# Kernel optimization log

Measured on AMD Instinct MI355X. Metric: run time of the kernel, lower is better.

## Reference

```python
import jax, jax.numpy as jnp
import numpy as np

EPS = 1e-5
DN = ('NCHW', 'OIHW', 'NCHW')

def conv(x, w, b, stride, pad):
    y = jax.lax.conv_general_dilated(x, w, (stride, stride), [(pad, pad), (pad, pad)], dimension_numbers=DN)
    return y + b[None, :, None, None]

def instance_norm(x, gamma, beta):
    # normalize over spatial dims per (N, C)
    mu = jnp.mean(x, axis=(2, 3), keepdims=True)
    var = jnp.var(x, axis=(2, 3), keepdims=True)
    xh = (x - mu) * jax.lax.rsqrt(var + EPS)
    return xh * gamma[None, :, None, None] + beta[None, :, None, None]

def lrelu(x):
    return jnp.where(x >= 0, x, 0.2 * x)

def block(x, w, b, g, be, stride, pad):
    return lrelu(instance_norm(conv(x, w, b, stride, pad), g, be))

def setup_inputs() -> dict:
    key = jax.random.key(0)
    ks = jax.random.split(key, 16)
    dim = 64
    def rn(k, shape, s=0.05):
        return jax.random.normal(k, shape, dtype=jnp.float32) * s
    inp = {
        'x':   jax.random.normal(ks[0], (256, 3, 64, 64), dtype=jnp.float32),
        'w1': rn(ks[1], (dim, 3, 5, 5)),        'b1': jnp.zeros((dim,), jnp.float32),
        'g1': jnp.ones((dim,), jnp.float32),    'be1': jnp.zeros((dim,), jnp.float32),
        'w2': rn(ks[2], (dim*2, dim, 5, 5)),    'b2': jnp.zeros((dim*2,), jnp.float32),
        'g2': jnp.ones((dim*2,), jnp.float32),  'be2': jnp.zeros((dim*2,), jnp.float32),
        'w3': rn(ks[3], (dim*4, dim*2, 5, 5)),  'b3': jnp.zeros((dim*4,), jnp.float32),
        'g3': jnp.ones((dim*4,), jnp.float32),  'be3': jnp.zeros((dim*4,), jnp.float32),
        'w4': rn(ks[4], (dim*4, dim*4, 3, 3)),  'b4': jnp.zeros((dim*4,), jnp.float32),
        'g4': jnp.ones((dim*4,), jnp.float32),  'be4': jnp.zeros((dim*4,), jnp.float32),
        # MBD tensor T: (in_features=4096, out_features=64, kernel_dims=50), init N(0,1)
        'T':  jax.random.normal(ks[5], (4096, 64, 50), dtype=jnp.float32),
        'fc_w': rn(ks[6], (1000, 4096 + 64), s=0.02),
        'fc_b': jnp.zeros((1000,), jnp.float32),
    }
    return inp

def reference(x, w1, b1, g1, be1, w2, b2, g2, be2, w3, b3, g3, be3, w4, b4, g4, be4, T, fc_w, fc_b):
    bs = x.shape[0]
    f = block(x, w1, b1, g1, be1, 2, 2)   # (bs,64,32,32)
    f = block(f, w2, b2, g2, be2, 2, 2)   # (bs,128,16,16)
    f = block(f, w3, b3, g3, be3, 2, 2)   # (bs,256,8,8)
    f = block(f, w4, b4, g4, be4, 2, 1)   # (bs,256,4,4)
    feat = f.reshape(bs, -1)              # (bs,4096)
    # minibatch discrimination
    M = jnp.einsum('bi,iok->bok', feat, T)          # (bs,64,50)
    norm = jnp.sum(jnp.abs(M[None] - M[:, None]), axis=3)  # (bs,bs,64); [i,j]=|M_i-M_j|
    o_b = jnp.sum(jnp.exp(-norm), axis=0) - 1.0     # (bs,64)
    mb = jnp.concatenate([feat, o_b], axis=1)       # (bs,4160)
    y = mb @ fc_w.T + fc_b                          # (bs,1000)
    return feat, y
```

## Files before the change

### kernel.cpp

```cpp
#include <hip/hip_runtime.h>
#include <hip/hip_fp16.h>
#include <math.h>

#define EPSF 1e-5f

typedef __attribute__((ext_vector_type(4))) float  floatx4;
typedef __attribute__((ext_vector_type(4))) short  short4v;
typedef __attribute__((ext_vector_type(8))) short  short8v;

__device__ __forceinline__ unsigned short cvt_bf16(float f){
  unsigned u = __float_as_uint(f);
  unsigned r = (u + 0x7FFFu + ((u >> 16) & 1u)) >> 16;
  return (unsigned short)r;
}
__device__ __forceinline__ float bf2f(unsigned short h){
  return __uint_as_float(((unsigned)h) << 16);
}
__device__ __forceinline__ short8v ld_frag(const unsigned short* p){
  short4v lo = *(const short4v*)p;
  short4v hi = *(const short4v*)(p + 4);
  return __builtin_shufflevector(lo, hi, 0,1,2,3,4,5,6,7);
}
__device__ __forceinline__ float lrelu(float x){ return x >= 0.f ? x : 0.2f*x; }

__global__ __launch_bounds__(256) void prep_k(const float* __restrict__ w1, const float* __restrict__ w2,
                                              const float* __restrict__ w3, const float* __restrict__ w4,
                                              unsigned short* __restrict__ wb1, unsigned short* __restrict__ wb2,
                                              unsigned short* __restrict__ wb3, unsigned short* __restrict__ wb4,
                                              float* __restrict__ SQ){
  int b = blockIdx.x, t = threadIdx.x;
  if (b < 32){
    int idx = b*256 + t;
    int j = idx&7, lane = (idx>>3)&63, ks = (idx>>9)&3, grp = idx>>11;
    int co = grp*16 + (lane&15);
    int k = ks*32 + ((lane>>4)<<3) + j;
    int tap6 = k>>2, ci = k&3;
    int kh = tap6/6, kw = tap6 - kh*6;
    float v = 0.f;
    if (ci < 3 && kh < 5 && kw < 5) v = w1[(co*3 + ci)*25 + kh*5 + kw];
    wb1[idx] = cvt_bf16(v);
  } else if (b < 832){
    int idx = (b-32)*256 + t;
    int grp = idx/25600, rem = idx - grp*25600;
    int tap = rem/1024, rem2 = rem - tap*1024;
    int ccg = rem2>>9, lane = (rem2>>3)&63, j = rem2&7;
    int co = grp*16 + (lane&15);
    int ci = ccg*32 + ((lane>>4)<<3) + j;
    wb2[idx] = cvt_bf16(w2[(co*64 + ci)*25 + tap]);
  } else if (b < 4032){
    int idx = (b-832)*256 + t;
    int grp = idx/51200, rem = idx - grp*51200;
    int tap = rem/2048, rem2 = rem - tap*2048;
    int ccg = rem2>>9, lane = (rem2>>3)&63, j = rem2&7;
    int co = grp*16 + (lane&15);
    int ci = ccg*32 + ((lane>>4)<<3) + j;
    wb3[idx] = cvt_bf16(w3[(co*128 + ci)*25 + tap]);
  } else if (b < 6336){
    int idx = (b-4032)*256 + t;
    int grp = idx/36864, rem = idx - grp*36864;
    int tap = rem/4096, rem2 = rem - tap*4096;
    int ccg = rem2>>9, lane = (rem2>>3)&63, j = rem2&7;
    int co = grp*16 + (lane&15);
    int ci = ccg*32 + ((lane>>4)<<3) + j;
    wb4[idx] = cvt_bf16(w4[(co*256 + ci)*9 + tap]);
  } else {
    int idx = (b-6336)*256 + t;
    SQ[idx] = 0.f;
  }
}

__global__ __launch_bounds__(256) void conv1_k(const float* __restrict__ x, const unsigned short* __restrict__ wb1P,
                                               float* __restrict__ S1, float* __restrict__ Q1,
                                               unsigned short* __restrict__ f1raw){
  const int t = threadIdx.x, n = blockIdx.x>>1, half = blockIdx.x&1;
  const int w = t>>6, lane = t&63, q = lane>>4, l16 = lane&15;
  __shared__ __align__(16) unsigned short img[36*68*4];
  short8v bf[4][4];
  #pragma unroll
  for (int nt=0;nt<4;nt++)
    #pragma unroll
    for (int ks=0;ks<4;ks++)
      bf[nt][ks] = *(const short8v*)&wb1P[((nt*4+ks)*64 + lane)*8];
  for (int i=t; i<4896; i+=256) ((unsigned*)img)[i] = 0u;
  __syncthreads();
  for (int idx=t; idx<1680; idx+=256){
    int ci = idx/560, rem = idx - ci*560;
    int tih = rem>>4, iw4 = (rem&15)<<2;
    int ih = half*32 - 2 + tih;
    if ((unsigned)ih < 64u){
      float4 v = *(const float4*)&x[((n*3+ci)<<12) + (ih<<6) + iw4];
      int base = (tih*68 + iw4 + 2)*4 + ci;
      img[base]    = cvt_bf16(v.x);
      img[base+4]  = cvt_bf16(v.y);
      img[base+8]  = cvt_bf16(v.z);
      img[base+12] = cvt_bf16(v.w);
    }
  }
  __syncthreads();
  floatx4 acc[8][4];
  #pragma unroll
  for (int mi=0;mi<8;mi++)
    #pragma unroll
    for (int nt=0;nt<4;nt++) acc[mi][nt] = (floatx4){0.f,0.f,0.f,0.f};
  #pragma unroll
  for (int mi=0; mi<8; mi++){
    int r = w*8 + mi;
    int ohl = r>>1, ow = ((r&1)<<4) + l16;
    #pragma unroll
    for (int ks=0; ks<4; ks++){
      int t0 = ks*8 + 2*q;
      int kh = t0/6, kw = t0 - kh*6;
      short8v a = ld_frag(&img[((ohl*2+kh)*68 + ow*2 + kw)*4]);
      #pragma unroll
      for (int nt=0; nt<4; nt++)
        acc[mi][nt] = __builtin_amdgcn_mfma_f32_16x16x32_bf16(a, bf[nt][ks], acc[mi][nt], 0,0,0);
    }
  }
  float sreg[4] = {0,0,0,0}, qreg[4] = {0,0,0,0};
  #pragma unroll
  for (int mi=0;mi<8;mi++){
    int r = w*8 + mi;
    #pragma unroll
    for (int nt=0;nt<4;nt++)
      #pragma unroll
      for (int e=0;e<4;e++){
        float v = acc[mi][nt][e];
        sreg[nt] += v; qreg[nt] += v*v;
        int px = half*512 + (r<<4) + (q<<2) + e;
        f1raw[(((n<<10)+px)<<6) + (nt<<4) + l16] = cvt_bf16(v);
      }
  }
  #pragma unroll
  for (int nt=0;nt<4;nt++){
    float s = sreg[nt], qq = qreg[nt];
    s  += __shfl_xor(s,16,64);  s  += __shfl_xor(s,32,64);
    qq += __shfl_xor(qq,16,64); qq += __shfl_xor(qq,32,64);
    if (q==0){
      atomicAdd(&S1[(n<<6) + (nt<<4) + l16], s);
      atomicAdd(&Q1[(n<<6) + (nt<<4) + l16], qq);
    }
  }
}

__global__ __launch_bounds__(256) void conv2_k(const unsigned short* __restrict__ fin,
                                               const unsigned short* __restrict__ wbP,
                                               const float* __restrict__ S1, const float* __restrict__ Q1,
                                               const float* __restrict__ g1, const float* __restrict__ be1,
                                               float* __restrict__ S2, float* __restrict__ Q2,
                                               unsigned short* __restrict__ fout){
  const int t = threadIdx.x;
  const int n = blockIdx.x >> 1, half = blockIdx.x & 1;
  const int w = t>>6, lane = t&63, q = lane>>4, l16 = lane&15;
  const int rw = w&1, cw = w>>1;
  __shared__ __align__(16) unsigned short tile[684*40];
  __shared__ float gmA[64], btA[64];
  if (t < 64){
    float S = S1[(n<<6)+t], Q = Q1[(n<<6)+t];
    float mu = S*(1.f/1024.f), var = fmaxf(Q*(1.f/1024.f) - mu*mu, 0.f);
    float r = rsqrtf(var+EPSF)*g1[t];
    gmA[t] = r; btA[t] = be1[t] - mu*r;
  }
  __syncthreads();
  floatx4 acc[4][4];
  #pragma unroll
  for (int mt=0;mt<4;mt++)
    #pragma unroll
    for (int nt=0;nt<4;nt++) acc[mt][nt] = (floatx4){0.f,0.f,0.f,0.f};
  int cellb[4];
  #pragma unroll
  for (int mt=0;mt<4;mt++){
    int r = rw*64 + mt*16 + l16;
    int ohl = r>>4, ow = r&15;
    cellb[mt] = (2*ohl)*36 + 2*ow;
  }
  for (int ccg = 0; ccg < 2; ccg++){
    const int cc = ccg<<5;
    if (ccg) __syncthreads();
    #pragma unroll
    for (int it=0; it<11; it++){
      int idx = it*256 + t;
      if (idx < 2736){
        int cell = idx>>2, ci0 = (idx&3)<<3;
        int tih = cell/36, tiw = cell - tih*36;
        int ih = half*16 + tih - 2, iw = tiw - 2;
        uint4 v = {0u,0u,0u,0u};
        if ((unsigned)ih < 32u && (unsigned)iw < 32u){
          v = *(const uint4*)&fin[(((n*32+ih)*32 + iw)<<6) + cc + ci0];
          unsigned short* hp = (unsigned short*)&v;
          #pragma unroll
          for (int jj=0;jj<8;jj++){
            int c = cc + ci0 + jj;
            hp[jj] = cvt_bf16(lrelu(bf2f(hp[jj])*gmA[c]+btA[c]));
          }
        }
        *(uint4*)&tile[cell*40 + ci0] = v;
      }
    }
    __syncthreads();
    const unsigned short* bp[4];
    #pragma unroll
    for (int nt=0;nt<4;nt++)
      bp[nt] = wbP + ((((cw*4+nt)*25)*2 + ccg)<<9) + lane*8;
    short8v bcur[4];
    #pragma unroll
    for (int nt=0;nt<4;nt++) bcur[nt] = *(const short8v*)bp[nt];
    for (int tap=0; tap<25; tap++){
      int tn = tap+1 < 25 ? tap+1 : tap;
      short8v bnx[4];
      #pragma unroll
      for (int nt=0;nt<4;nt++) bnx[nt] = *(const short8v*)(bp[nt] + (tn<<10));
      int kh = tap/5, kw = tap - kh*5;
      int aoff = kh*36 + kw;
      short8v a[4];
      #pragma unroll
      for (int mt=0;mt<4;mt++) a[mt] = *(const short8v*)&tile[(cellb[mt]+aoff)*40 + q*8];
      #pragma unroll
      for (int mt=0;mt<4;mt++)
        #pragma unroll
        for (int nt=0;nt<4;nt++)
          acc[mt][nt] = __builtin_amdgcn_mfma_f32_16x16x32_bf16(a[mt], bcur[nt], acc[mt][nt], 0,0,0);
      #pragma unroll
      for (int nt=0;nt<4;nt++) bcur[nt] = bnx[nt];
    }
  }
  #pragma unroll
  for (int nt=0;nt<4;nt++){
    int co = cw*64 + nt*16 + l16;
    float s=0.f, qq=0.f;
    #pragma unroll
    for (int mt=0;mt<4;mt++)
      #pragma unroll
      for (int e=0;e<4;e++){ float xv = acc[mt][nt][e]; s += xv; qq += xv*xv; }
    s  += __shfl_xor(s,16,64);  s  += __shfl_xor(s,32,64);
    qq += __shfl_xor(qq,16,64); qq += __shfl_xor(qq,32,64);
    if (q == 0){
      atomicAdd(&S2[n*128 + co], s);
      atomicAdd(&Q2[n*128 + co], qq);
    }
    #pragma unroll
    for (int mt=0;mt<4;mt++)
      #pragma unroll
      for (int e=0;e<4;e++){
        int px = half*128 + rw*64 + mt*16 + q*4 + e;
        fout[((n<<8) + px)*128 + co] = cvt_bf16(acc[mt][nt][e]);
      }
  }
}

__global__ __launch_bounds__(256) void conv3_k(const unsigned short* __restrict__ fin,
                                               const unsigned short* __restrict__ wbP,
                                               const float* __restrict__ S2, const float* __restrict__ Q2,
                                               const float* __restrict__ g2, const float* __restrict__ be2,
                                               const float* __restrict__ g, const float* __restrict__ be,
                                               unsigned short* __restrict__ fout){
  const int t = threadIdx.x, n = blockIdx.x, co0 = blockIdx.y<<7;
  const int w = t>>6, lane = t&63, q = lane>>4, l16 = lane&15;
  const int rw = w&1, cw = w>>1;
  __shared__ __align__(16) unsigned short tile[361*40];
  __shared__ float gmA[128], btA[128];
  __shared__ float SQs[2][128], SQq[2][128];
  if (t < 128){
    float S = S2[n*128+t], Q = Q2[n*128+t];
    float mu = S*(1.f/256.f), var = fmaxf(Q*(1.f/256.f) - mu*mu, 0.f);
    float r = rsqrtf(var+EPSF)*g2[t];
    gmA[t] = r; btA[t] = be2[t] - mu*r;
  }
  __syncthreads();
  floatx4 acc[2][4];
  #pragma unroll
  for (int mt=0;mt<2;mt++)
    #pragma unroll
    for (int nt=0;nt<4;nt++) acc[mt][nt] = (floatx4){0.f,0.f,0.f,0.f};
  int cellb[2];
  #pragma unroll
  for (int mt=0;mt<2;mt++){
    int r = rw*32 + mt*16 + l16;
    int oh = r>>3, ow = r&7;
    cellb[mt] = (2*oh)*19 + 2*ow;
  }
  for (int ccg = 0; ccg < 4; ccg++){
    const int cc = ccg<<5;
    if (ccg) __syncthreads();
    #pragma unroll
    for (int it=0; it<6; it++){
      int idx = it*256 + t;
      if (idx < 1444){
        int cell = idx>>2, ci0 = (idx&3)<<3;
        int tih = cell/19, tiw = cell - tih*19;
        int ih = tih - 2, iw = tiw - 2;
        uint4 v = {0u,0u,0u,0u};
        if ((unsigned)ih < 16u && (unsigned)iw < 16u){
          v = *(const uint4*)&fin[(((n*16+ih)*16 + iw)<<7) + cc + ci0];
          unsigned short* hp = (unsigned short*)&v;
          #pragma unroll
          for (int jj=0;jj<8;jj++){
            int c = cc + ci0 + jj;
            hp[jj] = cvt_bf16(lrelu(bf2f(hp[jj])*gmA[c]+btA[c]));
          }
        }
        *(uint4*)&tile[cell*40 + ci0] = v;
      }
    }
    __syncthreads();
    const unsigned short* bp[4];
    #pragma unroll
    for (int nt=0;nt<4;nt++)
      bp[nt] = wbP + (((((co0>>4)+cw*4+nt)*25)*4 + ccg)<<9) + lane*8;
    short8v bcur[4];
    #pragma unroll
    for (int nt=0;nt<4;nt++) bcur[nt] = *(const short8v*)bp[nt];
    for (int tap=0; tap<25; tap++){
      int tn = tap+1 < 25 ? tap+1 : tap;
      short8v bnx[4];
      #pragma unroll
      for (int nt=0;nt<4;nt++) bnx[nt] = *(const short8v*)(bp[nt] + (tn<<11));
      int kh = tap/5, kw = tap - kh*5;
      int aoff = kh*19 + kw;
      short8v a[2];
      #pragma unroll
      for (int mt=0;mt<2;mt++) a[mt] = *(const short8v*)&tile[(cellb[mt]+aoff)*40 + q*8];
      #pragma unroll
      for (int mt=0;mt<2;mt++)
        #pragma unroll
        for (int nt=0;nt<4;nt++)
          acc[mt][nt] = __builtin_amdgcn_mfma_f32_16x16x32_bf16(a[mt], bcur[nt], acc[mt][nt], 0,0,0);
      #pragma unroll
      for (int nt=0;nt<4;nt++) bcur[nt] = bnx[nt];
    }
  }
  #pragma unroll
  for (int nt=0;nt<4;nt++){
    int lcol = cw*64 + nt*16 + l16;
    float s=0.f, qq=0.f;
    #pragma unroll
    for (int mt=0;mt<2;mt++)
      #pragma unroll
      for (int e=0;e<4;e++){ float xv = acc[mt][nt][e]; s += xv; qq += xv*xv; }
    s  += __shfl_xor(s,16,64);  s  += __shfl_xor(s,32,64);
    qq += __shfl_xor(qq,16,64); qq += __shfl_xor(qq,32,64);
    if (q == 0){ SQs[rw][lcol] = s; SQq[rw][lcol] = qq; }
  }
  __syncthreads();
  #pragma unroll
  for (int nt=0;nt<4;nt++){
    int lcol = cw*64 + nt*16 + l16, co = co0 + lcol;
    float S = SQs[0][lcol] + SQs[1][lcol];
    float Q = SQq[0][lcol] + SQq[1][lcol];
    float mu = S*(1.f/64.f), var = fmaxf(Q*(1.f/64.f) - mu*mu, 0.f);
    float gmv = rsqrtf(var+EPSF)*g[co];
    float btv = be[co] - mu*gmv;
    #pragma unroll
    for (int mt=0;mt<2;mt++)
      #pragma unroll
      for (int e=0;e<4;e++){
        int row = rw*32 + mt*16 + q*4 + e;
        fout[((n<<6) + row)*256 + co] = cvt_bf16(lrelu(acc[mt][nt][e]*gmv+btv));
      }
  }
}

__global__ __launch_bounds__(256) void conv4_k(const unsigned short* __restrict__ fin,
                                               const unsigned short* __restrict__ wbP,
                                               const float* __restrict__ g, const float* __restrict__ be,
                                               float* __restrict__ feat, unsigned short* __restrict__ featb){
  const int t = threadIdx.x;
  const int n0 = blockIdx.x << 1, co0 = blockIdx.y << 6;
  const int w = t>>6, lane = t&63, q = lane>>4, l16 = lane&15;
  const int rw = w&1, cw = w>>1;
  __shared__ __align__(16) unsigned short tile[2*81*40];
  floatx4 acc[2];
  acc[0] = (floatx4){0.f,0.f,0.f,0.f};
  acc[1] = (floatx4){0.f,0.f,0.f,0.f};
  const int oh = l16>>2, ow = l16&3;
  const int cellb = (2*oh)*9 + 2*ow;
  for (int ccg = 0; ccg < 8; ccg++){
    const int cc = ccg<<5;
    if (ccg) __syncthreads();
    #pragma unroll
    for (int it=0; it<3; it++){
      int idx = it*256 + t;
      if (idx < 648){
        int img = idx >= 324 ? 1 : 0;
        int rem = idx - img*324;
        int cell = rem>>2, ci0 = (rem&3)<<3;
        int tih = cell/9, tiw = cell - tih*9;
        int ih = tih - 1, iw = tiw - 1;
        uint4 v = {0u,0u,0u,0u};
        if ((unsigned)ih < 8u && (unsigned)iw < 8u)
          v = *(const uint4*)&fin[((((n0+img)*8+ih)*8 + iw)<<8) + cc + ci0];
        *(uint4*)&tile[(img*81+cell)*40 + ci0] = v;
      }
    }
    __syncthreads();
    const unsigned short* bp[2];
    #pragma unroll
    for (int nt=0;nt<2;nt++)
      bp[nt] = wbP + (((((co0>>4)+cw*2+nt)*9)*8 + ccg)<<9) + lane*8;
    short8v bcur[2];
    #pragma unroll
    for (int nt=0;nt<2;nt++) bcur[nt] = *(const short8v*)bp[nt];
    for (int tap=0; tap<9; tap++){
      int tn = tap+1 < 9 ? tap+1 : tap;
      short8v bnx[2];
      #pragma unroll
      for (int nt=0;nt<2;nt++) bnx[nt] = *(const short8v*)(bp[nt] + (tn<<12));
      int kh = tap/3, kw = tap - kh*3;
      short8v a = *(const short8v*)&tile[(rw*81 + cellb + kh*9 + kw)*40 + q*8];
      #pragma unroll
      for (int nt=0;nt<2;nt++)
        acc[nt] = __builtin_amdgcn_mfma_f32_16x16x32_bf16(a, bcur[nt], acc[nt], 0,0,0);
      bcur[0] = bnx[0]; bcur[1] = bnx[1];
    }
  }
  const int nn = n0 + rw;
  #pragma unroll
  for (int nt=0;nt<2;nt++){
    int co = co0 + cw*32 + nt*16 + l16;
    float s=0.f, qq=0.f;
    #pragma unroll
    for (int e=0;e<4;e++){ float xv = acc[nt][e]; s += xv; qq += xv*xv; }
    s  += __shfl_xor(s,16,64);  s  += __shfl_xor(s,32,64);
    qq += __shfl_xor(qq,16,64); qq += __shfl_xor(qq,32,64);
    float mu = s*(1.f/16.f), var = fmaxf(qq*(1.f/16.f) - mu*mu, 0.f);
    float gmv = rsqrtf(var+EPSF)*g[co];
    float btv = be[co] - mu*gmv;
    #pragma unroll
    for (int e=0;e<4;e++){
      int px = q*4 + e;
      float vv = lrelu(acc[nt][e]*gmv+btv);
      feat [(nn<<12) + (co<<4) + px] = vv;
      featb[(nn<<12) + (co<<4) + px] = cvt_bf16(vv);
    }
  }
}

__global__ __launch_bounds__(256) void gemmM_k(const unsigned short* __restrict__ A,
                                               const float* __restrict__ T,
                                               float* __restrict__ Cp){
  const int t = threadIdx.x;
  const int n0 = blockIdx.x<<7, b0 = blockIdx.y<<7, k0 = blockIdx.z<<9;
  const int w = t>>6, lane = t&63, q = lane>>4, l16 = lane&15;
  const int rw = w&1, cw = w>>1;
  __shared__ __align__(16) unsigned short Asm[128*40];
  __shared__ __align__(16) unsigned short Bsm[128*40];
  floatx4 acc[4][4];
  #pragma unroll
  for (int mt=0;mt<4;mt++)
    #pragma unroll
    for (int nt=0;nt<4;nt++) acc[mt][nt] = (floatx4){0.f,0.f,0.f,0.f};
  for (int kk=0; kk<512; kk+=32){
    if (kk) __syncthreads();
    #pragma unroll
    for (int m=0;m<2;m++){
      int idx = t + (m<<8);
      int row = idx>>2, seg = idx&3;
      uint4 v = *(const uint4*)&A[(b0+row)*4096 + k0 + kk + (seg<<3)];
      *(uint4*)&Asm[row*40 + (seg<<3)] = v;
    }
    #pragma unroll
    for (int m=0;m<4;m++){
      int idx = t + (m<<8);
      int kr = idx>>5, ns = (idx&31)<<2;
      float4 v = *(const float4*)&T[(k0+kk+kr)*3200 + n0 + ns];
      Bsm[(ns+0)*40 + kr] = cvt_bf16(v.x);
      Bsm[(ns+1)*40 + kr] = cvt_bf16(v.y);
      Bsm[(ns+2)*40 + kr] = cvt_bf16(v.z);
      Bsm[(ns+3)*40 + kr] = cvt_bf16(v.w);
    }
    __syncthreads();
    short8v af[4], bfr[4];
    #pragma unroll
    for (int mt=0;mt<4;mt++) af[mt] = *(const short8v*)&Asm[((rw<<6)+(mt<<4)+l16)*40 + (q<<3)];
    #pragma unroll
    for (int nt=0;nt<4;nt++) bfr[nt] = *(const short8v*)&Bsm[((cw<<6)+(nt<<4)+l16)*40 + (q<<3)];
    #pragma unroll
    for (int mt=0;mt<4;mt++)
      #pragma unroll
      for (int nt=0;nt<4;nt++)
        acc[mt][nt] = __builtin_amdgcn_mfma_f32_16x16x32_bf16(af[mt], bfr[nt], acc[mt][nt], 0,0,0);
  }
  float* C = Cp + blockIdx.z * 819200;
  #pragma unroll
  for (int mt=0;mt<4;mt++)
    #pragma unroll
    for (int nt=0;nt<4;nt++)
      #pragma unroll
      for (int e=0;e<4;e++){
        int row = b0 + (rw<<6) + (mt<<4) + (q<<2) + e;
        int col = n0 + (cw<<6) + (nt<<4) + l16;
        C[row*3200 + col] = acc[mt][nt][e];
      }
}

__global__ __launch_bounds__(256) void reduceM_k(const float* __restrict__ Cp, __half* __restrict__ Mh){
  int idx = blockIdx.x*256 + threadIdx.x;
  if (idx >= 851968) return;
  int i = idx / 3328, r = idx - i*3328;
  int o = r / 52, k = r - o*52;
  float v = 0.f;
  if (k < 50){
    int src = i*3200 + o*50 + k;
    #pragma unroll
    for (int s = 0; s < 8; s++) v += Cp[s*819200 + src];
  }
  Mh[idx] = __float2half(v);
}

__global__ __launch_bounds__(256) void pair_k(const __half* __restrict__ Mh,
                                              float* __restrict__ ob, unsigned short* __restrict__ obb){
  const int j = blockIdx.x, t = threadIdx.x;
  __shared__ __align__(16) __half2 Mj[1664];
  __shared__ float red[256];
  for (int k=t; k<1664; k+=256) Mj[k] = *(const __half2*)&Mh[j*3328 + (k<<1)];
  __syncthreads();
  const int o = t & 63, ss = t >> 6;
  const __half2* mjp = &Mj[o*26];
  float sum = 0.f;
  for (int i = ss<<6; i < (ss<<6)+64; i++){
    const __half2* mip = (const __half2*)&Mh[i*3328 + o*52];
    __half2 acch = __float2half2_rn(0.f);
    #pragma unroll
    for (int k2=0;k2<26;k2++){
      __half2 d = __hsub2(mip[k2], mjp[k2]);
      acch = __hadd2(acch, __habs2(d));
    }
    float dsum = __low2float(acch) + __high2float(acch);
    sum += __expf(-dsum);
  }
  red[(o<<2)+ss] = sum;
  __syncthreads();
  if (t < 64){
    float v = red[t<<2] + red[(t<<2)+1] + red[(t<<2)+2] + red[(t<<2)+3] - 1.0f;
    ob[(j<<6)+t] = v;
    obb[(j<<6)+t] = cvt_bf16(v);
  }
}

__global__ __launch_bounds__(256) void gemmFC_k(const unsigned short* __restrict__ featb,
                                                const unsigned short* __restrict__ obb,
                                                const float* __restrict__ W, float* __restrict__ Cp){
  const int t = threadIdx.x;
  const int o0 = blockIdx.x<<7, b0 = blockIdx.y<<7, k0 = blockIdx.z*320;
  const int w = t>>6, lane = t&63, q = lane>>4, l16 = lane&15;
  const int rw = w&1, cw = w>>1;
  __shared__ __align__(16) unsigned short Asm[128*40];
  __shared__ __align__(16) unsigned short Bsm[128*40];
  floatx4 acc[4][4];
  #pragma unroll
  for (int mt=0;mt<4;mt++)
    #pragma unroll
    for (int nt=0;nt<4;nt++) acc[mt][nt] = (floatx4){0.f,0.f,0.f,0.f};
  for (int kk=0; kk<320; kk+=32){
    if (kk) __syncthreads();
    #pragma unroll
    for (int m=0;m<2;m++){
      int idx = t + (m<<8);
      int row = idx>>2, seg = idx&3;
      int i = k0 + kk + (seg<<3);
      uint4 v;
      if (i < 4096) v = *(const uint4*)&featb[(b0+row)*4096 + i];
      else          v = *(const uint4*)&obb[(b0+row)*64 + (i-4096)];
      *(uint4*)&Asm[row*40 + (seg<<3)] = v;
    }
    #pragma unroll
    for (int m=0;m<4;m++){
      int idx = t + (m<<8);
      int orow = idx>>3, seg = idx&7;
      int oo = o0 + orow;
      float4 v = {0,0,0,0};
      if (oo < 1000) v = *(const float4*)&W[oo*4160 + k0 + kk + (seg<<2)];
      unsigned short h[4] = {cvt_bf16(v.x), cvt_bf16(v.y), cvt_bf16(v.z), cvt_bf16(v.w)};
      *(uint2*)&Bsm[orow*40 + (seg<<2)] = *(uint2*)h;
    }
    __syncthreads();
    short8v af[4], bfr[4];
    #pragma unroll
    for (int mt=0;mt<4;mt++) af[mt] = *(const short8v*)&Asm[((rw<<6)+(mt<<4)+l16)*40 + (q<<3)];
    #pragma unroll
    for (int nt=0;nt<4;nt++) bfr[nt] = *(const short8v*)&Bsm[((cw<<6)+(nt<<4)+l16)*40 + (q<<3)];
    #pragma unroll
    for (int mt=0;mt<4;mt++)
      #pragma unroll
      for (int nt=0;nt<4;nt++)
        acc[mt][nt] = __builtin_amdgcn_mfma_f32_16x16x32_bf16(af[mt], bfr[nt], acc[mt][nt], 0,0,0);
  }
  float* C = Cp + blockIdx.z * 256000;
  #pragma unroll
  for (int mt=0;mt<4;mt++)
    #pragma unroll
    for (int nt=0;nt<4;nt++)
      #pragma unroll
      for (int e=0;e<4;e++){
        int row = b0 + (rw<<6) + (mt<<4) + (q<<2) + e;
        int col = o0 + (cw<<6) + (nt<<4) + l16;
        if (col < 1000) C[row*1000 + col] = acc[mt][nt][e];
      }
}

__global__ __launch_bounds__(256) void reduceY_k(const float* __restrict__ Cp, const float* __restrict__ bias,
                                                 float* __restrict__ y){
  int idx = blockIdx.x * 256 + threadIdx.x;
  if (idx >= 256000) return;
  int o = idx % 1000;
  float r = bias[o];
  #pragma unroll
  for (int s = 0; s < 13; s++) r += Cp[s*256000 + idx];
  y[idx] = r;
}

extern "C" void kernel_launch(void* const* d_in, const int* in_sizes, int n_in,
                              void* d_out, int out_size, void* d_ws, size_t ws_size,
                              hipStream_t stream){
  const float* x   = (const float*)d_in[0];
  const float* w1  = (const float*)d_in[1];
  const float* g1  = (const float*)d_in[3];
  const float* be1 = (const float*)d_in[4];
  const float* w2  = (const float*)d_in[5];
  const float* g2  = (const float*)d_in[7];
  const float* be2 = (const float*)d_in[8];
  const float* w3  = (const float*)d_in[9];
  const float* g3  = (const float*)d_in[11];
  const float* be3 = (const float*)d_in[12];
  const float* w4  = (const float*)d_in[13];
  const float* g4  = (const float*)d_in[15];
  const float* be4 = (const float*)d_in[16];
  const float* T   = (const float*)d_in[17];
  const float* fcw = (const float*)d_in[18];
  const float* fcb = (const float*)d_in[19];
  float* out = (float*)d_out;
  float* ws  = (float*)d_ws;

  unsigned short* f1raw = (unsigned short*)ws;
  unsigned short* f2    = (unsigned short*)(ws + 8388608);
  unsigned short* f3    = (unsigned short*)(ws + 12582912);
  unsigned short* featb = (unsigned short*)(ws + 14680064);
  unsigned short* wb1   = (unsigned short*)(ws + 15204352);
  unsigned short* wb2   = (unsigned short*)(ws + 15208448);
  unsigned short* wb3   = (unsigned short*)(ws + 15310848);
  unsigned short* wb4   = (unsigned short*)(ws + 15720448);
  float* S1    = ws + 16015360;
  float* Q1    = ws + 16031744;
  float* S2    = ws + 16048128;
  float* Q2    = ws + 16080896;
  float* Mp    = ws + 16113664;
  __half* Mh   = (__half*)(ws + 22667264);
  float* obuf  = ws + 23093248;
  unsigned short* obb = (unsigned short*)(ws + 23109632);
  float* yp    = ws + 23117824;
  float* feat  = out;
  float* y     = out + 1048576;

  prep_k<<<dim3(6720), 256, 0, stream>>>(w1, w2, w3, w4, wb1, wb2, wb3, wb4, S1);

  conv1_k<<<dim3(512),     256, 0, stream>>>(x, wb1, S1, Q1, f1raw);
  conv2_k<<<dim3(512),     256, 0, stream>>>(f1raw, wb2, S1, Q1, g1, be1, S2, Q2, f2);
  conv3_k<<<dim3(256, 2),  256, 0, stream>>>(f2, wb3, S2, Q2, g2, be2, g3, be3, f3);
  conv4_k<<<dim3(128, 4),  256, 0, stream>>>(f3, wb4, g4, be4, feat, featb);

  gemmM_k  <<<dim3(25, 2, 8),  256, 0, stream>>>(featb, T, Mp);
  reduceM_k<<<dim3(3328),      256, 0, stream>>>(Mp, Mh);
  pair_k   <<<dim3(256),       256, 0, stream>>>(Mh, obuf, obb);
  gemmFC_k <<<dim3(8, 2, 13),  256, 0, stream>>>(featb, obb, fcw, yp);
  reduceY_k<<<dim3(1000),      256, 0, stream>>>(yp, fcb, y);
}
```

Measured before the change: 367.2 us.

## Prepack T and fc weights into MFMA fragment layout, drop LDS staging

Adds packT_k and packW_k kernels that convert T and fc_w to bf16 in the exact per-lane MFMA fragment order, reusing dead workspace regions (f1raw, Mp). gemmM_k and gemmFC_k then load A and B fragments directly from global memory without shared-memory staging or barriers, and without per-tile fp32-to-bf16 conversion and transposed scalar LDS stores. This costs two extra launches and a full extra read/write pass over T (about 52 MB in) and fc_w each call. The GEMMs also lose LDS reuse, so each fragment is fetched from global or L2 by more waves.

```diff
diff --git a/kernel.cpp b/kernel.cpp
--- a/kernel.cpp
+++ b/kernel.cpp
@@ -69,6 +69,49 @@
   }
 }
 
+__global__ __launch_bounds__(256) void packT_k(const float* __restrict__ T,
+                                               unsigned short* __restrict__ Tp){
+  const int b = blockIdx.x, t = threadIdx.x;
+  __shared__ float tile[32][133];
+  const int nb = b % 25, kt = b / 25;
+  const int n0 = nb*128, k0 = kt*32;
+  #pragma unroll
+  for (int m=0;m<4;m++){
+    int idx = m*256 + t;
+    int row = idx>>5, c4 = (idx&31)<<2;
+    const float4 v = *(const float4*)&T[(k0+row)*3200 + n0 + c4];
+    tile[row][c4]   = v.x; tile[row][c4+1] = v.y;
+    tile[row][c4+2] = v.z; tile[row][c4+3] = v.w;
+  }
+  __syncthreads();
+  #pragma unroll
+  for (int m=0;m<2;m++){
+    int c = m*256 + t;
+    int ngl = c>>6, lane = c&63, q = lane>>4, r = lane&15;
+    unsigned short h[8];
+    #pragma unroll
+    for (int j=0;j<8;j++) h[j] = cvt_bf16(tile[q*8+j][ngl*16 + r]);
+    *(uint4*)&Tp[(((nb*8 + ngl)*128 + kt)*64 + lane)*8] = *(const uint4*)h;
+  }
+}
+
+__global__ __launch_bounds__(256) void packW_k(const float* __restrict__ W,
+                                               unsigned short* __restrict__ Wp){
+  int idx = blockIdx.x*256 + threadIdx.x;
+  int lane = idx & 63, rem = idx >> 6;
+  int kt = rem % 130, ng = rem / 130;
+  int q = lane>>4, r = lane&15;
+  int orow = ng*16 + r, k = kt*32 + (q<<3);
+  unsigned short h[8] = {0,0,0,0,0,0,0,0};
+  if (orow < 1000){
+    float4 v0 = *(const float4*)&W[orow*4160 + k];
+    float4 v1 = *(const float4*)&W[orow*4160 + k + 4];
+    h[0]=cvt_bf16(v0.x); h[1]=cvt_bf16(v0.y); h[2]=cvt_bf16(v0.z); h[3]=cvt_bf16(v0.w);
+    h[4]=cvt_bf16(v1.x); h[5]=cvt_bf16(v1.y); h[6]=cvt_bf16(v1.z); h[7]=cvt_bf16(v1.w);
+  }
+  *(uint4*)&Wp[idx*8] = *(const uint4*)h;
+}
+
 __global__ __launch_bounds__(256) void conv1_k(const float* __restrict__ x, const unsigned short* __restrict__ wb1P,
                                                float* __restrict__ S1, float* __restrict__ Q1,
                                                unsigned short* __restrict__ f1raw){
@@ -435,44 +478,32 @@
 }
 
 __global__ __launch_bounds__(256) void gemmM_k(const unsigned short* __restrict__ A,
-                                               const float* __restrict__ T,
+                                               const unsigned short* __restrict__ Tp,
                                                float* __restrict__ Cp){
   const int t = threadIdx.x;
   const int n0 = blockIdx.x<<7, b0 = blockIdx.y<<7, k0 = blockIdx.z<<9;
   const int w = t>>6, lane = t&63, q = lane>>4, l16 = lane&15;
   const int rw = w&1, cw = w>>1;
-  __shared__ __align__(16) unsigned short Asm[128*40];
-  __shared__ __align__(16) unsigned short Bsm[128*40];
   floatx4 acc[4][4];
   #pragma unroll
   for (int mt=0;mt<4;mt++)
     #pragma unroll
     for (int nt=0;nt<4;nt++) acc[mt][nt] = (floatx4){0.f,0.f,0.f,0.f};
-  for (int kk=0; kk<512; kk+=32){
-    if (kk) __syncthreads();
-    #pragma unroll
-    for (int m=0;m<2;m++){
-      int idx = t + (m<<8);
-      int row = idx>>2, seg = idx&3;
-      uint4 v = *(const uint4*)&A[(b0+row)*4096 + k0 + kk + (seg<<3)];
-      *(uint4*)&Asm[row*40 + (seg<<3)] = v;
-    }
-    #pragma unroll
-    for (int m=0;m<4;m++){
-      int idx = t + (m<<8);
-      int kr = idx>>5, ns = (idx&31)<<2;
-      float4 v = *(const float4*)&T[(k0+kk+kr)*3200 + n0 + ns];
-      Bsm[(ns+0)*40 + kr] = cvt_bf16(v.x);
-      Bsm[(ns+1)*40 + kr] = cvt_bf16(v.y);
-      Bsm[(ns+2)*40 + kr] = cvt_bf16(v.z);
-      Bsm[(ns+3)*40 + kr] = cvt_bf16(v.w);
-    }
-    __syncthreads();
+  const unsigned short* Ab[4];
+  const unsigned short* Bb[4];
+  #pragma unroll
+  for (int mt=0;mt<4;mt++)
+    Ab[mt] = A + (b0 + (rw<<6) + (mt<<4) + l16)*4096 + k0 + (q<<3);
+  #pragma unroll
+  for (int nt=0;nt<4;nt++)
+    Bb[nt] = Tp + ((((n0>>4) + (cw<<2) + nt)*128 + (k0>>5))*64 + lane)*8;
+  #pragma unroll 4
+  for (int kt=0; kt<16; kt++){
     short8v af[4], bfr[4];
     #pragma unroll
-    for (int mt=0;mt<4;mt++) af[mt] = *(const short8v*)&Asm[((rw<<6)+(mt<<4)+l16)*40 + (q<<3)];
-    #pragma unroll
-    for (int nt=0;nt<4;nt++) bfr[nt] = *(const short8v*)&Bsm[((cw<<6)+(nt<<4)+l16)*40 + (q<<3)];
+    for (int mt=0;mt<4;mt++) af[mt] = *(const short8v*)(Ab[mt] + kt*32);
+    #pragma unroll
+    for (int nt=0;nt<4;nt++) bfr[nt] = *(const short8v*)(Bb[nt] + kt*512);
     #pragma unroll
     for (int mt=0;mt<4;mt++)
       #pragma unroll
@@ -538,46 +569,34 @@
 
 __global__ __launch_bounds__(256) void gemmFC_k(const unsigned short* __restrict__ featb,
                                                 const unsigned short* __restrict__ obb,
-                                                const float* __restrict__ W, float* __restrict__ Cp){
+                                                const unsigned short* __restrict__ Wp,
+                                                float* __restrict__ Cp){
   const int t = threadIdx.x;
-  const int o0 = blockIdx.x<<7, b0 = blockIdx.y<<7, k0 = blockIdx.z*320;
+  const int o0 = blockIdx.x<<7, b0 = blockIdx.y<<7, kz = blockIdx.z;
   const int w = t>>6, lane = t&63, q = lane>>4, l16 = lane&15;
   const int rw = w&1, cw = w>>1;
-  __shared__ __align__(16) unsigned short Asm[128*40];
-  __shared__ __align__(16) unsigned short Bsm[128*40];
   floatx4 acc[4][4];
   #pragma unroll
   for (int mt=0;mt<4;mt++)
     #pragma unroll
     for (int nt=0;nt<4;nt++) acc[mt][nt] = (floatx4){0.f,0.f,0.f,0.f};
-  for (int kk=0; kk<320; kk+=32){
-    if (kk) __syncthreads();
-    #pragma unroll
-    for (int m=0;m<2;m++){
-      int idx = t + (m<<8);
-      int row = idx>>2, seg = idx&3;
-      int i = k0 + kk + (seg<<3);
-      uint4 v;
-      if (i < 4096) v = *(const uint4*)&featb[(b0+row)*4096 + i];
-      else          v = *(const uint4*)&obb[(b0+row)*64 + (i-4096)];
-      *(uint4*)&Asm[row*40 + (seg<<3)] = v;
-    }
-    #pragma unroll
-    for (int m=0;m<4;m++){
-      int idx = t + (m<<8);
-      int orow = idx>>3, seg = idx&7;
-      int oo = o0 + orow;
-      float4 v = {0,0,0,0};
-      if (oo < 1000) v = *(const float4*)&W[oo*4160 + k0 + kk + (seg<<2)];
-      unsigned short h[4] = {cvt_bf16(v.x), cvt_bf16(v.y), cvt_bf16(v.z), cvt_bf16(v.w)};
-      *(uint2*)&Bsm[orow*40 + (seg<<2)] = *(uint2*)h;
-    }
-    __syncthreads();
+  int rowb[4];
+  #pragma unroll
+  for (int mt=0;mt<4;mt++) rowb[mt] = b0 + (rw<<6) + (mt<<4) + l16;
+  const unsigned short* Bb[4];
+  #pragma unroll
+  for (int nt=0;nt<4;nt++)
+    Bb[nt] = Wp + ((((o0>>4) + (cw<<2) + nt)*130 + kz*10)*64 + lane)*8;
+  #pragma unroll 2
+  for (int kt=0; kt<10; kt++){
+    int k = kz*320 + kt*32 + (q<<3);
     short8v af[4], bfr[4];
     #pragma unroll
-    for (int mt=0;mt<4;mt++) af[mt] = *(const short8v*)&Asm[((rw<<6)+(mt<<4)+l16)*40 + (q<<3)];
-    #pragma unroll
-    for (int nt=0;nt<4;nt++) bfr[nt] = *(const short8v*)&Bsm[((cw<<6)+(nt<<4)+l16)*40 + (q<<3)];
+    for (int mt=0;mt<4;mt++)
+      af[mt] = (k < 4096) ? *(const short8v*)&featb[rowb[mt]*4096 + k]
+                          : *(const short8v*)&obb[rowb[mt]*64 + (k-4096)];
+    #pragma unroll
+    for (int nt=0;nt<4;nt++) bfr[nt] = *(const short8v*)(Bb[nt] + kt*512);
     #pragma unroll
     for (int mt=0;mt<4;mt++)
       #pragma unroll
@@ -631,6 +650,7 @@
   float* ws  = (float*)d_ws;
 
   unsigned short* f1raw = (unsigned short*)ws;
+  unsigned short* Tp    = (unsigned short*)ws;
   unsigned short* f2    = (unsigned short*)(ws + 8388608);
   unsigned short* f3    = (unsigned short*)(ws + 12582912);
   unsigned short* featb = (unsigned short*)(ws + 14680064);
@@ -643,6 +663,7 @@
   float* S2    = ws + 16048128;
   float* Q2    = ws + 16080896;
   float* Mp    = ws + 16113664;
+  unsigned short* Wp  = (unsigned short*)(ws + 16113664);
   __half* Mh   = (__half*)(ws + 22667264);
   float* obuf  = ws + 23093248;
   unsigned short* obb = (unsigned short*)(ws + 23109632);
@@ -654,12 +675,14 @@
 
   conv1_k<<<dim3(512),     256, 0, stream>>>(x, wb1, S1, Q1, f1raw);
   conv2_k<<<dim3(512),     256, 0, stream>>>(f1raw, wb2, S1, Q1, g1, be1, S2, Q2, f2);
+  packT_k<<<dim3(3200),    256, 0, stream>>>(T, Tp);
   conv3_k<<<dim3(256, 2),  256, 0, stream>>>(f2, wb3, S2, Q2, g2, be2, g3, be3, f3);
   conv4_k<<<dim3(128, 4),  256, 0, stream>>>(f3, wb4, g4, be4, feat, featb);
 
-  gemmM_k  <<<dim3(25, 2, 8),  256, 0, stream>>>(featb, T, Mp);
+  gemmM_k  <<<dim3(25, 2, 8),  256, 0, stream>>>(featb, Tp, Mp);
   reduceM_k<<<dim3(3328),      256, 0, stream>>>(Mp, Mh);
+  packW_k  <<<dim3(2080),      256, 0, stream>>>(fcw, Wp);
   pair_k   <<<dim3(256),       256, 0, stream>>>(Mh, obuf, obb);
-  gemmFC_k <<<dim3(8, 2, 13),  256, 0, stream>>>(featb, obb, fcw, yp);
+  gemmFC_k <<<dim3(8, 2, 13),  256, 0, stream>>>(featb, obb, Wp, yp);
   reduceY_k<<<dim3(1000),      256, 0, stream>>>(yp, fcb, y);
 }
```

Result: faster. 349.2 us (-4.9%).
